# Kernel optimization log

Measured on AMD Instinct MI355X. Metric: run time of the kernel, lower is better.

## Reference

```python
import jax, jax.numpy as jnp
import numpy as np

NPOINT = 2048
RADIUS = 0.4
NSAMPLE = 32
EPS = 1e-5  # BatchNorm eps


def setup_inputs() -> dict:
    key = jax.random.key(0)
    ks = jax.random.split(key, 16)
    B, N, Cf = 8, 8192, 6
    xyz = jax.random.uniform(ks[0], (B, 3, N), jnp.float32)        # coords in unit cube
    points = jax.random.normal(ks[1], (B, Cf, N), jnp.float32)     # per-point features
    inp = {"xyz": xyz, "points": points}
    dims = [9, 64, 64, 128]  # in_channel=3+Cf, mlp=[64,64,128]
    for i in range(3):
        cin, cout = dims[i], dims[i + 1]
        bound = 1.0 / np.sqrt(cin)
        inp[f"w{i+1}"] = jax.random.uniform(ks[2 + 4 * i], (cout, cin), jnp.float32, -bound, bound)
        inp[f"b{i+1}"] = jax.random.uniform(ks[3 + 4 * i], (cout,), jnp.float32, -bound, bound)
        inp[f"g{i+1}"] = jnp.ones((cout,), jnp.float32)   # BN gamma
        inp[f"be{i+1}"] = jnp.zeros((cout,), jnp.float32)  # BN beta
    return inp


def _fps(pts):
    """Furthest point sampling. pts: (N,3) -> (NPOINT,) int32 indices (first index is 0)."""
    N = pts.shape[0]

    def step(carry, _):
        dist, last = carry
        d = jnp.sum((pts - pts[last]) ** 2, axis=-1)
        dist = jnp.minimum(dist, d)
        nxt = jnp.argmax(dist).astype(jnp.int32)
        return (dist, nxt), last

    init = (jnp.full((N,), 1e10, pts.dtype), jnp.int32(0))
    _, idx = jax.lax.scan(step, init, None, length=NPOINT)
    return idx


def _ball_query(new_xyz_t, xyz_t):
    """Indices of up to NSAMPLE points within RADIUS of each centroid; empty slots
    replicate the first in-ball index (pointnet2_ops semantics).
    new_xyz_t: (B,S,3), xyz_t: (B,N,3) -> (B,S,NSAMPLE) int32."""
    N = xyz_t.shape[1]
    sq = jnp.sum((new_xyz_t[:, :, None, :] - xyz_t[:, None, :, :]) ** 2, axis=-1)  # (B,S,N)
    mask = sq <= RADIUS ** 2
    # key = own index if in ball else N -> stable argsort yields in-ball indices in order
    keys = jnp.where(mask, jnp.arange(N, dtype=jnp.int32), jnp.int32(N))
    order = jnp.argsort(keys, axis=-1)[..., :NSAMPLE].astype(jnp.int32)            # (B,S,K)
    cnt = jnp.sum(mask, axis=-1)                                                   # (B,S)
    valid = jnp.arange(NSAMPLE, dtype=jnp.int32)[None, None, :] < cnt[..., None]
    return jnp.where(valid, order, order[..., :1])


def _forward(xyz, points, params):
    xyz_t = jnp.transpose(xyz, (0, 2, 1))          # (B,N,3)
    pts_t = jnp.transpose(points, (0, 2, 1))       # (B,N,C)

    fps_idx = jax.vmap(_fps)(xyz_t)                # (B,S)
    gather = jax.vmap(lambda p, i: p[i])
    new_xyz_t = gather(xyz_t, fps_idx)             # (B,S,3)

    idx = _ball_query(new_xyz_t, xyz_t)            # (B,S,K)
    grouped_xyz = gather(xyz_t, idx) - new_xyz_t[:, :, None, :]   # (B,S,K,3) centered
    grouped_pts = gather(pts_t, idx)                              # (B,S,K,C)
    feat = jnp.concatenate([grouped_xyz, grouped_pts], axis=-1)   # (B,S,K,3+C)
    x = jnp.transpose(feat, (0, 3, 1, 2))                         # (B,Cin,S,K)

    for (w, b, g, be) in params:
        x = jnp.einsum('oc,bcsk->bosk', w, x) + b[None, :, None, None]  # 1x1 conv
        mu = jnp.mean(x, axis=(0, 2, 3), keepdims=True)                  # BN (batch stats)
        var = jnp.mean((x - mu) ** 2, axis=(0, 2, 3), keepdims=True)
        x = (x - mu) * jax.lax.rsqrt(var + EPS) * g[None, :, None, None] + be[None, :, None, None]
        x = jax.nn.relu(x)

    new_points = jnp.max(x, axis=-1)               # (B,D,S) max over nsample
    new_xyz = jnp.transpose(new_xyz_t, (0, 2, 1))  # (B,3,S)
    return new_xyz, new_points


def reference(xyz, points, w1, b1, g1, be1, w2, b2, g2, be2, w3, b3, g3, be3):
    params = [(w1, b1, g1, be1), (w2, b2, g2, be2), (w3, b3, g3, be3)]
    return _forward(xyz, points, params)
```

## Files before the change

kernel.cpp:

```cpp
#include <hip/hip_runtime.h>
#include <cstdint>

#define N_PTS   8192
#define S_PTS   2048
#define K_SMP   32
#define BATCH   8
#define P_TOT   (BATCH*S_PTS*K_SMP)
#define R2      0.16f
#define CNT_INV (1.0f/524288.0f)

__device__ __forceinline__ float sqd(float ax, float ay, float az,
                                     float bx, float by, float bz) {
    float dx = __fsub_rn(ax, bx), dy = __fsub_rn(ay, by), dz = __fsub_rn(az, bz);
    return __fadd_rn(__fadd_rn(__fmul_rn(dx, dx), __fmul_rn(dy, dy)), __fmul_rn(dz, dz));
}

#define ROR_STEP(N)                                                                         \
    {                                                                                       \
        float ov = __int_as_float(__builtin_amdgcn_mov_dpp(__float_as_int(bv),              \
                                                           0x120|(N), 0xF, 0xF, true));     \
        int   oi = __builtin_amdgcn_mov_dpp(bi, 0x120|(N), 0xF, 0xF, true);                 \
        if (ov > bv || (ov == bv && oi < bi)) { bv = ov; bi = oi; }                         \
    }

__global__ __launch_bounds__(256) void fps_kernel(const float* __restrict__ xyz,
                                                  float* __restrict__ newxyz) {
    __shared__ float sx[N_PTS], sy[N_PTS], sz[N_PTS];
    __shared__ unsigned long long s_part[2][16];
    __shared__ int s_sel[S_PTS];

    const int b = blockIdx.x, t = threadIdx.x;
    const float* xb = xyz + (size_t)b * 3 * N_PTS;
    const int base = t * 32;

    float px[32], py[32], pz[32], dist[32];
#pragma unroll
    for (int q = 0; q < 8; q++) {
        float4 vx = *(const float4*)(xb + base + 4 * q);
        float4 vy = *(const float4*)(xb + N_PTS + base + 4 * q);
        float4 vz = *(const float4*)(xb + 2 * N_PTS + base + 4 * q);
        px[4*q] = vx.x; px[4*q+1] = vx.y; px[4*q+2] = vx.z; px[4*q+3] = vx.w;
        py[4*q] = vy.x; py[4*q+1] = vy.y; py[4*q+2] = vy.z; py[4*q+3] = vy.w;
        pz[4*q] = vz.x; pz[4*q+1] = vz.y; pz[4*q+2] = vz.z; pz[4*q+3] = vz.w;
    }
#pragma unroll
    for (int j = 0; j < 32; j++) {
        sx[base+j] = px[j]; sy[base+j] = py[j]; sz[base+j] = pz[j];
        dist[j] = 1e10f;
    }
    if (t == 0) s_sel[0] = 0;
    __syncthreads();

    int last = 0;
    for (int i = 1; i < S_PTS; i++) {
        float lx = sx[last], ly = sy[last], lz = sz[last];
        float mv = -1.0f;
#pragma unroll
        for (int j = 0; j < 32; j++) {
            float d  = sqd(px[j], py[j], pz[j], lx, ly, lz);
            float nd = fminf(dist[j], d);
            dist[j] = nd;
            mv = fmaxf(mv, nd);
        }
        int mi = base;
#pragma unroll
        for (int j = 31; j >= 0; j--) if (dist[j] == mv) mi = base + j;

        float bv = mv; int bi = mi;
        ROR_STEP(1) ROR_STEP(2) ROR_STEP(4) ROR_STEP(8)
        if ((t & 15) == 0)
            s_part[i & 1][t >> 4] =
                ((unsigned long long)__float_as_uint(bv) << 32)
                | (unsigned long long)(0xFFFFFFFFu - (unsigned)bi);
        __syncthreads();
        unsigned long long best = s_part[i & 1][0];
#pragma unroll
        for (int r = 1; r < 16; r++) {
            unsigned long long k = s_part[i & 1][r];
            if (k > best) best = k;
        }
        last = (int)(0xFFFFFFFFu - (unsigned)(best & 0xFFFFFFFFull)) & (N_PTS - 1);
        if (t == 0) s_sel[i] = last;
    }
    __syncthreads();
    for (int s = t; s < S_PTS; s += 256) {
        int id = s_sel[s];
        newxyz[((size_t)b*3 + 0) * S_PTS + s] = sx[id];
        newxyz[((size_t)b*3 + 1) * S_PTS + s] = sy[id];
        newxyz[((size_t)b*3 + 2) * S_PTS + s] = sz[id];
    }
}

__global__ __launch_bounds__(256) void ball_kernel(const float* __restrict__ xyz,
                                                   const float* __restrict__ newxyz,
                                                   int* __restrict__ ballidx) {
    int g    = blockIdx.x * 4 + (threadIdx.x >> 6);
    int lane = threadIdx.x & 63;
    int b = g >> 11, s = g & 2047;
    const float* xb = xyz + (size_t)b * 3 * N_PTS;
    float cx = newxyz[((size_t)b*3 + 0) * S_PTS + s];
    float cy = newxyz[((size_t)b*3 + 1) * S_PTS + s];
    float cz = newxyz[((size_t)b*3 + 2) * S_PTS + s];
    int* outp = ballidx + (size_t)g * K_SMP;

    int cnt = 0, first = 0;  bool have_first = false;
    for (int n0 = 0; n0 < N_PTS; n0 += 64) {
        int n = n0 + lane;
        float d = sqd(cx, cy, cz, xb[n], xb[N_PTS + n], xb[2*N_PTS + n]);
        bool in = (d <= R2);
        unsigned long long m = __ballot(in);
        if (in) {
            int pos = cnt + __popcll(m & ((1ull << lane) - 1ull));
            if (pos < K_SMP) outp[pos] = n;
        }
        if (!have_first && m != 0ull) { first = n0 + (int)__builtin_ctzll(m); have_first = true; }
        cnt += __popcll(m);
        if (cnt >= K_SMP) break;
    }
    if (cnt < K_SMP && lane < K_SMP && lane >= cnt) outp[lane] = first;
}

__global__ __launch_bounds__(256) void d_conv1(const float* __restrict__ xyz,
                                               const float* __restrict__ points,
                                               const float* __restrict__ newxyz,
                                               const int* __restrict__ ballidx,
                                               const float* __restrict__ w1,
                                               const float* __restrict__ b1,
                                               float* __restrict__ xbuf) {
    __shared__ float sw[64 * 9];
    __shared__ float sb[64];
    int t = threadIdx.x;
    for (int i = t; i < 576; i += 256) sw[i] = w1[i];
    if (t < 64) sb[t] = b1[t];
    __syncthreads();

    int p = blockIdx.x * 256 + t;
    int g = p >> 5, b = g >> 11, s = g & 2047;
    int idx = ballidx[p] & (N_PTS - 1);
    const float* xb = xyz    + (size_t)b * 3 * N_PTS;
    const float* pb = points + (size_t)b * 6 * N_PTS;
    float f[9];
    f[0] = xb[idx]           - newxyz[((size_t)b*3 + 0) * S_PTS + s];
    f[1] = xb[N_PTS + idx]   - newxyz[((size_t)b*3 + 1) * S_PTS + s];
    f[2] = xb[2*N_PTS + idx] - newxyz[((size_t)b*3 + 2) * S_PTS + s];
#pragma unroll
    for (int c = 0; c < 6; c++) f[3 + c] = pb[c * N_PTS + idx];

    float* row = xbuf + (size_t)p * 64;
    for (int co = 0; co < 64; co++) {
        float a = sb[co];
#pragma unroll
        for (int c = 0; c < 9; c++) a += sw[co * 9 + c] * f[c];
        row[co] = a;
    }
}

template <int C>
__global__ __launch_bounds__(256) void d_stats(const float* __restrict__ x,
                                               float* __restrict__ gstat) {
    __shared__ float ss[C], sq[C];
    int t = threadIdx.x;
    for (int i = t; i < C; i += 256) { ss[i] = 0.f; sq[i] = 0.f; }
    __syncthreads();
    int c = t & (C - 1), r0 = t / C;
    const int RPI = 256 / C;
    float s = 0.f, q = 0.f;
    size_t base = (size_t)blockIdx.x * 256;
    for (int r = r0; r < 256; r += RPI) {
        float v = x[(base + r) * C + c];
        s += v; q += v * v;
    }
    atomicAdd(&ss[c], s); atomicAdd(&sq[c], q);
    __syncthreads();
    for (int i = t; i < C; i += 256) { atomicAdd(&gstat[i], ss[i]); atomicAdd(&gstat[C + i], sq[i]); }
}

__global__ __launch_bounds__(256) void c2_kernel(float* __restrict__ xbuf,
                                                 const float* __restrict__ AB1,
                                                 const float* __restrict__ w2,
                                                 const float* __restrict__ b2) {
    __shared__ __align__(16) float wt[64 * 64];
    __shared__ float sA[64], sB[64], sb[64];
    int t = threadIdx.x;
    for (int i = t; i < 4096; i += 256) { int co = i & 63, c = i >> 6; wt[c*64+co] = w2[co*64+c]; }
    if (t < 64) { sA[t] = AB1[t]; sB[t] = AB1[64 + t]; sb[t] = b2[t]; }
    __syncthreads();

    size_t p0 = (size_t)blockIdx.x * 512 + t, p1 = p0 + 256;
    float* r0 = xbuf + p0 * 64;
    float* r1 = xbuf + p1 * 64;

    float acc0[64], acc1[64];
#pragma unroll
    for (int co = 0; co < 64; co++) { float bv = sb[co]; acc0[co] = bv; acc1[co] = bv; }

#pragma unroll
    for (int c0 = 0; c0 < 64; c0 += 8) {
        float ya[8], yb[8];
#pragma unroll
        for (int q = 0; q < 8; q += 4) {
            float4 va = *(const float4*)(r0 + c0 + q);
            float4 vb = *(const float4*)(r1 + c0 + q);
            ya[q] = va.x; ya[q+1] = va.y; ya[q+2] = va.z; ya[q+3] = va.w;
            yb[q] = vb.x; yb[q+1] = vb.y; yb[q+2] = vb.z; yb[q+3] = vb.w;
        }
#pragma unroll
        for (int q = 0; q < 8; q++) {
            ya[q] = fmaxf(0.f, ya[q] * sA[c0+q] + sB[c0+q]);
            yb[q] = fmaxf(0.f, yb[q] * sA[c0+q] + sB[c0+q]);
        }
#pragma unroll
        for (int c = 0; c < 8; c++) {
            float fa = ya[c], fb = yb[c];
#pragma unroll
            for (int co = 0; co < 64; co += 4) {
                float4 w = *(const float4*)&wt[(c0+c)*64 + co];
                acc0[co]   += w.x * fa; acc0[co+1] += w.y * fa;
                acc0[co+2] += w.z * fa; acc0[co+3] += w.w * fa;
                acc1[co]   += w.x * fb; acc1[co+1] += w.y * fb;
                acc1[co+2] += w.z * fb; acc1[co+3] += w.w * fb;
            }
        }
    }
#pragma unroll
    for (int co = 0; co < 64; co += 4) {
        *(float4*)(r0 + co) = make_float4(acc0[co], acc0[co+1], acc0[co+2], acc0[co+3]);
        *(float4*)(r1 + co) = make_float4(acc1[co], acc1[co+1], acc1[co+2], acc1[co+3]);
    }
}

#define C3_COMPUTE(ACC)                                                                    \
    int quarter = t & 3, q = t >> 2, cb = quarter * 32;                                    \
    size_t pB = (size_t)blockIdx.x * 256 + q;                                              \
    const float* r0 = xbuf + (pB +   0) * 64;                                              \
    const float* r1 = xbuf + (pB +  64) * 64;                                              \
    const float* r2 = xbuf + (pB + 128) * 64;                                              \
    const float* r3 = xbuf + (pB + 192) * 64;                                              \
    float ACC[4][32];                                                                      \
    _Pragma("unroll")                                                                      \
    for (int co = 0; co < 32; co++) {                                                      \
        float bv = sb3[cb + co];                                                           \
        ACC[0][co] = bv; ACC[1][co] = bv; ACC[2][co] = bv; ACC[3][co] = bv;                \
    }                                                                                      \
    _Pragma("unroll")                                                                      \
    for (int c0 = 0; c0 < 64; c0 += 8) {                                                   \
        float y[4][8];                                                                     \
        _Pragma("unroll")                                                                  \
        for (int qq = 0; qq < 8; qq += 4) {                                                \
            float4 v0 = *(const float4*)(r0 + c0 + qq);                                    \
            float4 v1 = *(const float4*)(r1 + c0 + qq);                                    \
            float4 v2 = *(const float4*)(r2 + c0 + qq);                                    \
            float4 v3 = *(const float4*)(r3 + c0 + qq);                                    \
            y[0][qq] = v0.x; y[0][qq+1] = v0.y; y[0][qq+2] = v0.z; y[0][qq+3] = v0.w;      \
            y[1][qq] = v1.x; y[1][qq+1] = v1.y; y[1][qq+2] = v1.z; y[1][qq+3] = v1.w;      \
            y[2][qq] = v2.x; y[2][qq+1] = v2.y; y[2][qq+2] = v2.z; y[2][qq+3] = v2.w;      \
            y[3][qq] = v3.x; y[3][qq+1] = v3.y; y[3][qq+2] = v3.z; y[3][qq+3] = v3.w;      \
        }                                                                                  \
        _Pragma("unroll")                                                                  \
        for (int qq = 0; qq < 8; qq++) {                                                   \
            float A = sA[c0+qq], Bv = sB[c0+qq];                                           \
            y[0][qq] = fmaxf(0.f, y[0][qq] * A + Bv);                                      \
            y[1][qq] = fmaxf(0.f, y[1][qq] * A + Bv);                                      \
            y[2][qq] = fmaxf(0.f, y[2][qq] * A + Bv);                                      \
            y[3][qq] = fmaxf(0.f, y[3][qq] * A + Bv);                                      \
        }                                                                                  \
        _Pragma("unroll")                                                                  \
        for (int c = 0; c < 8; c++) {                                                      \
            float f0 = y[0][c], f1 = y[1][c], f2 = y[2][c], f3 = y[3][c];                  \
            _Pragma("unroll")                                                              \
            for (int co = 0; co < 32; co += 4) {                                           \
                float4 w = *(const float4*)&wt[(c0+c)*128 + cb + co];                      \
                ACC[0][co]   += w.x * f0; ACC[0][co+1] += w.y * f0;                        \
                ACC[0][co+2] += w.z * f0; ACC[0][co+3] += w.w * f0;                        \
                ACC[1][co]   += w.x * f1; ACC[1][co+1] += w.y * f1;                        \
                ACC[1][co+2] += w.z * f1; ACC[1][co+3] += w.w * f1;                        \
                ACC[2][co]   += w.x * f2; ACC[2][co+1] += w.y * f2;                        \
                ACC[2][co+2] += w.z * f2; ACC[2][co+3] += w.w * f2;                        \
                ACC[3][co]   += w.x * f3; ACC[3][co+1] += w.y * f3;                        \
                ACC[3][co+2] += w.z * f3; ACC[3][co+3] += w.w * f3;                        \
            }                                                                              \
        }                                                                                  \
    }

__global__ __launch_bounds__(256) void c3_stats(const float* __restrict__ xbuf,
                                                const float* __restrict__ AB2,
                                                const float* __restrict__ w3,
                                                const float* __restrict__ b3,
                                                float* __restrict__ gstat) {
    __shared__ __align__(16) float wt[64 * 128];
    __shared__ float sA[64], sB[64], sb3[128], ss[128], sq[128];
    int t = threadIdx.x;
    for (int i = t; i < 8192; i += 256) { int ch = i & 127, c = i >> 7; wt[c*128+ch] = w3[ch*64+c]; }
    if (t < 64) { sA[t] = AB2[t]; sB[t] = AB2[64 + t]; }
    if (t < 128) { sb3[t] = b3[t]; ss[t] = 0.f; sq[t] = 0.f; }
    __syncthreads();

    C3_COMPUTE(acc)

#pragma unroll
    for (int co = 0; co < 32; co++) {
        float s  = acc[0][co] + acc[1][co] + acc[2][co] + acc[3][co];
        float qq = acc[0][co]*acc[0][co] + acc[1][co]*acc[1][co]
                 + acc[2][co]*acc[2][co] + acc[3][co]*acc[3][co];
        atomicAdd(&ss[cb + co], s);
        atomicAdd(&sq[cb + co], qq);
    }
    __syncthreads();
    if (t < 128) { atomicAdd(&gstat[t], ss[t]); atomicAdd(&gstat[128 + t], sq[t]); }
}

__global__ __launch_bounds__(256) void c3_max(const float* __restrict__ xbuf,
                                              const float* __restrict__ AB2,
                                              const float* __restrict__ w3,
                                              const float* __restrict__ b3,
                                              const float* __restrict__ AB3,
                                              float* __restrict__ out_np) {
    __shared__ __align__(16) float wt[64 * 128];
    __shared__ float sA[64], sB[64], sb3[128], sA3[128], sB3[128];
    __shared__ unsigned int smax[8][128];
    int t = threadIdx.x;
    for (int i = t; i < 8192; i += 256) { int ch = i & 127, c = i >> 7; wt[c*128+ch] = w3[ch*64+c]; }
    if (t < 64) { sA[t] = AB2[t]; sB[t] = AB2[64 + t]; }
    if (t < 128) { sb3[t] = b3[t]; sA3[t] = AB3[t]; sB3[t] = AB3[128 + t]; }
    for (int i = t; i < 1024; i += 256) smax[i >> 7][i & 127] = 0u;
    __syncthreads();

    C3_COMPUTE(acc)

    int g0 = (q >> 5);
#pragma unroll
    for (int co = 0; co < 32; co++) {
        int ch = cb + co;
        float A = sA3[ch], Bv = sB3[ch];
        float v0 = fmaxf(0.f, acc[0][co] * A + Bv);
        float v1 = fmaxf(0.f, acc[1][co] * A + Bv);
        float v2 = fmaxf(0.f, acc[2][co] * A + Bv);
        float v3 = fmaxf(0.f, acc[3][co] * A + Bv);
        atomicMax(&smax[g0    ][ch], __float_as_uint(v0));
        atomicMax(&smax[g0 + 2][ch], __float_as_uint(v1));
        atomicMax(&smax[g0 + 4][ch], __float_as_uint(v2));
        atomicMax(&smax[g0 + 6][ch], __float_as_uint(v3));
    }
    __syncthreads();
    for (int i = t; i < 1024; i += 256) {
        int g = i >> 7, ch = i & 127;
        int G = blockIdx.x * 8 + g;
        int b = G >> 11, s = G & 2047;
        out_np[((size_t)b * 128 + ch) * 2048 + s] = __uint_as_float(smax[g][ch]);
    }
}

template <int C>
__global__ void finalize_kernel(const float* __restrict__ gstat,
                                const float* __restrict__ gamma,
                                const float* __restrict__ beta,
                                float* __restrict__ AB) {
    int t = threadIdx.x;
    if (t < C) {
        float mu  = gstat[t]     * CNT_INV;
        float ex2 = gstat[C + t] * CNT_INV;
        float var = ex2 - mu * mu;
        float A = gamma[t] * rsqrtf(var + 1e-5f);
        AB[t] = A; AB[C + t] = beta[t] - mu * A;
    }
}

extern "C" void kernel_launch(void* const* d_in, const int* in_sizes, int n_in,
                              void* d_out, int out_size, void* d_ws, size_t ws_size,
                              hipStream_t stream) {
    (void)in_sizes; (void)n_in; (void)out_size; (void)ws_size;
    const float* xyz    = (const float*)d_in[0];
    const float* points = (const float*)d_in[1];
    const float* w1 = (const float*)d_in[2],  *b1 = (const float*)d_in[3];
    const float* g1 = (const float*)d_in[4],  *be1 = (const float*)d_in[5];
    const float* w2 = (const float*)d_in[6],  *b2 = (const float*)d_in[7];
    const float* g2 = (const float*)d_in[8],  *be2 = (const float*)d_in[9];
    const float* w3 = (const float*)d_in[10], *b3 = (const float*)d_in[11];
    const float* g3 = (const float*)d_in[12], *be3 = (const float*)d_in[13];

    float* out    = (float*)d_out;
    float* out_np = out + (size_t)BATCH * 3 * S_PTS;

    char*  ws      = (char*)d_ws;
    int*   ballidx = (int*)ws;
    float* gbase   = (float*)(ws + (2ull << 20));
    float* gstat1  = gbase;
    float* gstat2  = gbase + 256;
    float* gstat3  = gbase + 512;
    float* AB1     = gbase + 768;
    float* AB2     = gbase + 896;
    float* AB3     = gbase + 1024;
    float* xbuf    = (float*)(ws + (4ull << 20));

    hipMemsetAsync(gstat1, 0, 768 * sizeof(float), stream);

    fps_kernel  <<<BATCH, 256, 0, stream>>>(xyz, out);
    ball_kernel <<<(BATCH * S_PTS) / 4, 256, 0, stream>>>(xyz, out, ballidx);
    d_conv1     <<<P_TOT / 256, 256, 0, stream>>>(xyz, points, out, ballidx, w1, b1, xbuf);
    d_stats<64> <<<P_TOT / 256, 256, 0, stream>>>(xbuf, gstat1);
    finalize_kernel<64><<<1, 64, 0, stream>>>(gstat1, g1, be1, AB1);
    c2_kernel   <<<P_TOT / 512, 256, 0, stream>>>(xbuf, AB1, w2, b2);
    d_stats<64> <<<P_TOT / 256, 256, 0, stream>>>(xbuf, gstat2);
    finalize_kernel<64><<<1, 64, 0, stream>>>(gstat2, g2, be2, AB2);
    c3_stats    <<<P_TOT / 256, 256, 0, stream>>>(xbuf, AB2, w3, b3, gstat3);
    finalize_kernel<128><<<1, 128, 0, stream>>>(gstat3, g3, be3, AB3);
    c3_max      <<<P_TOT / 256, 256, 0, stream>>>(xbuf, AB2, w3, b3, AB3, out_np);
}
```

Measured before the change: 3.468 ms.

## Widen FPS to 1024 threads with wave-level shuffle argmax and two-stage reduction

The furthest-point-sampling kernel now runs 1024 threads per batch, each holding 8 points instead of 32, which shortens the serial per-iteration distance update. The argmax now reduces across the full 64-lane wave with DPP and xor shuffles, then one wave reduces the 16 wave partials through shuffles. This cuts per-thread work on the sequential critical path but adds a second barrier per iteration and synchronisation across a larger block.

New measurement: 3.962 ms. +14.2%, slower.

```diff
diff --git a/kernel.cpp b/kernel.cpp
--- a/kernel.cpp
+++ b/kernel.cpp
@@ -22,20 +22,28 @@
         int   oi = __builtin_amdgcn_mov_dpp(bi, 0x120|(N), 0xF, 0xF, true);                 \
         if (ov > bv || (ov == bv && oi < bi)) { bv = ov; bi = oi; }                         \
     }
-
-__global__ __launch_bounds__(256) void fps_kernel(const float* __restrict__ xyz,
-                                                  float* __restrict__ newxyz) {
+#define XOR_STEP(N)                                                                         \
+    {                                                                                       \
+        float ov = __shfl_xor(bv, N);                                                       \
+        int   oi = __shfl_xor(bi, N);                                                       \
+        if (ov > bv || (ov == bv && oi < bi)) { bv = ov; bi = oi; }                         \
+    }
+
+__global__ __launch_bounds__(1024, 4) void fps_kernel(const float* __restrict__ xyz,
+                                                      float* __restrict__ newxyz) {
     __shared__ float sx[N_PTS], sy[N_PTS], sz[N_PTS];
     __shared__ unsigned long long s_part[2][16];
+    __shared__ unsigned long long s_best[2];
     __shared__ int s_sel[S_PTS];
 
     const int b = blockIdx.x, t = threadIdx.x;
+    const int w = t >> 6, lane = t & 63;
     const float* xb = xyz + (size_t)b * 3 * N_PTS;
-    const int base = t * 32;
-
-    float px[32], py[32], pz[32], dist[32];
-#pragma unroll
-    for (int q = 0; q < 8; q++) {
+    const int base = t * 8;
+
+    float px[8], py[8], pz[8], dist[8];
+#pragma unroll
+    for (int q = 0; q < 2; q++) {
         float4 vx = *(const float4*)(xb + base + 4 * q);
         float4 vy = *(const float4*)(xb + N_PTS + base + 4 * q);
         float4 vz = *(const float4*)(xb + 2 * N_PTS + base + 4 * q);
@@ -44,7 +52,7 @@
         pz[4*q] = vz.x; pz[4*q+1] = vz.y; pz[4*q+2] = vz.z; pz[4*q+3] = vz.w;
     }
 #pragma unroll
-    for (int j = 0; j < 32; j++) {
+    for (int j = 0; j < 8; j++) {
         sx[base+j] = px[j]; sy[base+j] = py[j]; sz[base+j] = pz[j];
         dist[j] = 1e10f;
     }
@@ -54,36 +62,35 @@
     int last = 0;
     for (int i = 1; i < S_PTS; i++) {
         float lx = sx[last], ly = sy[last], lz = sz[last];
-        float mv = -1.0f;
-#pragma unroll
-        for (int j = 0; j < 32; j++) {
+        float bv = -1.0f; int bi = 0;
+#pragma unroll
+        for (int j = 0; j < 8; j++) {
             float d  = sqd(px[j], py[j], pz[j], lx, ly, lz);
             float nd = fminf(dist[j], d);
             dist[j] = nd;
-            mv = fmaxf(mv, nd);
-        }
-        int mi = base;
-#pragma unroll
-        for (int j = 31; j >= 0; j--) if (dist[j] == mv) mi = base + j;
-
-        float bv = mv; int bi = mi;
+            if (nd > bv) { bv = nd; bi = base + j; }
+        }
         ROR_STEP(1) ROR_STEP(2) ROR_STEP(4) ROR_STEP(8)
-        if ((t & 15) == 0)
-            s_part[i & 1][t >> 4] =
-                ((unsigned long long)__float_as_uint(bv) << 32)
-                | (unsigned long long)(0xFFFFFFFFu - (unsigned)bi);
+        XOR_STEP(16) XOR_STEP(32)
+        if (lane == 0)
+            s_part[i & 1][w] = ((unsigned long long)__float_as_uint(bv) << 32)
+                             | (unsigned long long)(0xFFFFFFFFu - (unsigned)bi);
         __syncthreads();
-        unsigned long long best = s_part[i & 1][0];
-#pragma unroll
-        for (int r = 1; r < 16; r++) {
-            unsigned long long k = s_part[i & 1][r];
-            if (k > best) best = k;
-        }
-        last = (int)(0xFFFFFFFFu - (unsigned)(best & 0xFFFFFFFFull)) & (N_PTS - 1);
+        if (w == 0) {
+            unsigned long long k = s_part[i & 1][lane & 15];
+#pragma unroll
+            for (int off = 1; off <= 8; off <<= 1) {
+                unsigned long long ok = __shfl_xor(k, off);
+                if (ok > k) k = ok;
+            }
+            if (lane == 0) s_best[i & 1] = k;
+        }
+        __syncthreads();
+        last = (int)(0xFFFFFFFFu - (unsigned)(s_best[i & 1] & 0xFFFFFFFFull)) & (N_PTS - 1);
         if (t == 0) s_sel[i] = last;
     }
     __syncthreads();
-    for (int s = t; s < S_PTS; s += 256) {
+    for (int s = t; s < S_PTS; s += 1024) {
         int id = s_sel[s];
         newxyz[((size_t)b*3 + 0) * S_PTS + s] = sx[id];
         newxyz[((size_t)b*3 + 1) * S_PTS + s] = sy[id];
@@ -394,7 +401,7 @@
 
     hipMemsetAsync(gstat1, 0, 768 * sizeof(float), stream);
 
-    fps_kernel  <<<BATCH, 256, 0, stream>>>(xyz, out);
+    fps_kernel  <<<BATCH, 1024, 0, stream>>>(xyz, out);
     ball_kernel <<<(BATCH * S_PTS) / 4, 256, 0, stream>>>(xyz, out, ballidx);
     d_conv1     <<<P_TOT / 256, 256, 0, stream>>>(xyz, points, out, ballidx, w1, b1, xbuf);
     d_stats<64> <<<P_TOT / 256, 256, 0, stream>>>(xbuf, gstat1);
```
